# Kernel tuning notes

Hardware: AMD Instinct MI355X
Metric: run time of the kernel (lower is better)

## Reference

```python
import jax, jax.numpy as jnp
import numpy as np
from math import sqrt

NUM_HEADS = 16
DIM_MODEL = 1024


def setup_inputs() -> dict:
    key = jax.random.key(0)
    ks = jax.random.split(key, 12)
    B, S, D, M = 4, 1024, DIM_MODEL, 64
    bound = 1.0 / sqrt(D)
    def lin_w(k):
        return jax.random.uniform(k, (D, D), jnp.float32, -bound, bound)
    def lin_b(k):
        return jax.random.uniform(k, (D,), jnp.float32, -bound, bound)
    return {
        "query": jax.random.normal(ks[0], (B, S, D), jnp.float32),
        "key": jax.random.normal(ks[1], (B, S, D), jnp.float32),
        "value": jax.random.normal(ks[2], (B, S, D), jnp.float32),
        "mask": jax.random.randint(ks[3], (1, B, S, M), 0, 2).astype(jnp.float32),
        "Wq": lin_w(ks[4]), "bq": lin_b(ks[5]),
        "Wk": lin_w(ks[6]), "bk": lin_b(ks[7]),
        "Wv": lin_w(ks[8]), "bv": lin_b(ks[9]),
        "Wo": lin_w(ks[10]),
    }


def reference(query, key, value, mask, Wq, bq, Wk, bk, Wv, bv, Wo):
    B, S, D = query.shape
    H = NUM_HEADS
    d = D // H
    # projections + head split, permute(2,0,1,3) -> [H,B,S,d]
    q = (query @ Wq.T + bq).reshape(B, S, H, d).transpose(2, 0, 1, 3)
    k = (key @ Wk.T + bk).reshape(B, S, H, d).transpose(2, 0, 1, 3)
    v = (value @ Wv.T + bv).reshape(B, S, H, d).transpose(2, 0, 1, 3)
    attn = jnp.einsum("hbqd,hbkd->hbqk", q, k) / sqrt(d)  # [H,B,S,S]
    # custom mask: mask.repeat(H,1,1,1) then mask @ mask^T / sqrt(m).
    # Identical per-head, so compute once on [B,S,m] and broadcast over H.
    m2d = mask[0]  # [B,S,m]
    mm = jnp.einsum("bqm,bkm->bqk", m2d, m2d) / sqrt(m2d.shape[-1])
    attn = jnp.where(mm[None] == 0, jnp.float32(-1e9), attn)
    w = jax.nn.softmax(attn, axis=-1)  # dropout is identity in eval mode
    x = jnp.einsum("hbqk,hbkd->hbqd", w, v)  # [H,B,S,d]
    # torch: permute(1,2,0,3) -> [B,S,H,d]; transpose(1,2) -> [B,H,S,d];
    # contiguous().view(B,-1,H*d) -- row-major reshape (mixes head/seq layout, replicated faithfully)
    x = jnp.transpose(x, (1, 0, 2, 3))  # [B,H,S,d]
    x = x.reshape(B, -1, H * d)
    return x @ Wo.T
```

## Files before the change

### kernel.cpp

```cpp
#include <hip/hip_runtime.h>

typedef unsigned int u32;
typedef unsigned short u16;
typedef unsigned long long u64;
typedef __attribute__((ext_vector_type(8))) short s16x8;
typedef __attribute__((ext_vector_type(8))) __bf16 bf16x8;
typedef __attribute__((ext_vector_type(4))) float f32x4;
typedef __attribute__((ext_vector_type(16))) float f32x16;
typedef __attribute__((ext_vector_type(4))) u32 u32x4;

#define WSMB (1ull << 20)
#define QSC 0.18033688011112042f

static __device__ __forceinline__ u16 f2bf(float f) {
  u32 u = __builtin_bit_cast(u32, f);
  return (u16)((u + 0x7fffu + ((u >> 16) & 1u)) >> 16);
}

static __device__ __forceinline__ u32 pkbf(float lo, float hi) {
  u32 r;
  asm("v_cvt_pk_bf16_f32 %0, %1, %2" : "=v"(r) : "v"(lo), "v"(hi));
  return r;
}

static __device__ __forceinline__ float ex2(float x) {
  float r;
  asm("v_exp_f32 %0, %1" : "=v"(r) : "v"(x));
  return r;
}

static __device__ __forceinline__ f32x4 mfma16x16(s16x8 a, s16x8 b, f32x4 c) {
  return __builtin_amdgcn_mfma_f32_16x16x32_bf16(
      __builtin_bit_cast(bf16x8, a), __builtin_bit_cast(bf16x8, b), c, 0, 0, 0);
}

static __device__ __forceinline__ f32x16 mfma32x32(s16x8 a, s16x8 b, f32x16 c) {
  return __builtin_amdgcn_mfma_f32_32x32x16_bf16(
      __builtin_bit_cast(bf16x8, a), __builtin_bit_cast(bf16x8, b), c, 0, 0, 0);
}

#define GLOAD_LDS16(g, l)                                                      \
  __builtin_amdgcn_global_load_lds(                                            \
      (const __attribute__((address_space(1))) u32*)(const void*)(g),          \
      (__attribute__((address_space(3))) u32*)(void*)(l), 16, 0, 0)

__global__ __launch_bounds__(256) void k_cvt3(const float* __restrict__ a,
                                              const float* __restrict__ b,
                                              const float* __restrict__ c,
                                              u16* __restrict__ oa,
                                              u16* __restrict__ ob,
                                              u16* __restrict__ oc) {
  const float* s;
  u16* d;
  if (blockIdx.y == 0) { s = a; d = oa; }
  else if (blockIdx.y == 1) { s = b; d = ob; }
  else { s = c; d = oc; }
  int i = (blockIdx.x * 256 + threadIdx.x) * 4;
  float4 v = *(const float4*)(s + i);
  u64 p = (u64)f2bf(v.x) | ((u64)f2bf(v.y) << 16) | ((u64)f2bf(v.z) << 32) |
          ((u64)f2bf(v.w) << 48);
  *(u64*)(d + i) = p;
}

__global__ __launch_bounds__(256) void k_cvt4(const float* __restrict__ a,
                                              const float* __restrict__ b,
                                              const float* __restrict__ c,
                                              const float* __restrict__ e,
                                              u16* __restrict__ oa,
                                              u16* __restrict__ ob,
                                              u16* __restrict__ oc,
                                              u16* __restrict__ oe) {
  const float* s;
  u16* d;
  if (blockIdx.y == 0) { s = a; d = oa; }
  else if (blockIdx.y == 1) { s = b; d = ob; }
  else if (blockIdx.y == 2) { s = c; d = oc; }
  else { s = e; d = oe; }
  int i = (blockIdx.x * 256 + threadIdx.x) * 4;
  float4 v = *(const float4*)(s + i);
  u64 p = (u64)f2bf(v.x) | ((u64)f2bf(v.y) << 16) | ((u64)f2bf(v.z) << 32) |
          ((u64)f2bf(v.w) << 48);
  *(u64*)(d + i) = p;
}

__global__ __launch_bounds__(256) void k_bits(const float* __restrict__ mask,
                                              u64* __restrict__ bits) {
  int w = threadIdx.x >> 6, l = threadIdx.x & 63;
  int r = blockIdx.x * 4 + w;
  float v = mask[(size_t)r * 64 + l];
  u64 bl = __ballot(v != 0.0f);
  if (l == 0) bits[r] = bl;
}

__global__ __launch_bounds__(256) void k_mm(const u64* __restrict__ bits,
                                            u64* __restrict__ MB) {
  int wv = threadIdx.x >> 6, l = threadIdx.x & 63;
  int qg = blockIdx.x * 4 + wv;
  u64 bq = bits[qg];
  const u64* bb = bits + (qg & ~1023);
  u64* out = MB + (size_t)qg * 16;
  for (int kt = 0; kt < 16; kt++) {
    u64 bk = bb[kt * 64 + l];
    u64 m = __ballot((bq & bk) != 0ull);
    if (l == 0) out[kt] = m;
  }
}

static __device__ __forceinline__ void gemm_core(const u16* __restrict__ A,
                                                 const u16* __restrict__ Bw,
                                                 f32x4 (&acc)[4][4]) {
  __shared__ __attribute__((aligned(16))) u16 As[2][4096];
  __shared__ __attribute__((aligned(16))) u16 Bs[2][4096];
  const int t = threadIdx.x;
  const int l = t & 63, w = t >> 6, lr = l & 15, lk = l >> 4;
  const int amr = (w & 1) * 64, bnr = (w >> 1) * 64;
  const int c0 = t, c1 = t + 256;
  const int r0 = c0 >> 2, r1 = c1 >> 2;
  const int sw0 = ((c0 & 3) * 8) ^ ((r0 & 6) << 2);
  const int sw1 = ((c1 & 3) * 8) ^ ((r1 & 6) << 2);
  const u16* Ag0 = A + (size_t)r0 * 1024 + sw0;
  const u16* Ag1 = A + (size_t)r1 * 1024 + sw1;
  const u16* Bg0 = Bw + (size_t)r0 * 1024 + sw0;
  const u16* Bg1 = Bw + (size_t)r1 * 1024 + sw1;
  const int aswz = (lk * 16) ^ ((lr & 6) << 3);

  GLOAD_LDS16(Ag0, &As[0][c0 * 8]);
  GLOAD_LDS16(Ag1, &As[0][c1 * 8]);
  GLOAD_LDS16(Bg0, &Bs[0][c0 * 8]);
  GLOAD_LDS16(Bg1, &Bs[0][c1 * 8]);

  int cur = 0;
  for (int kt = 0; kt < 1024; kt += 32) {
    __syncthreads();
    if (kt < 992) {
      const int nxt = cur ^ 1;
      GLOAD_LDS16(Ag0 + kt + 32, &As[nxt][c0 * 8]);
      GLOAD_LDS16(Ag1 + kt + 32, &As[nxt][c1 * 8]);
      GLOAD_LDS16(Bg0 + kt + 32, &Bs[nxt][c0 * 8]);
      GLOAD_LDS16(Bg1 + kt + 32, &Bs[nxt][c1 * 8]);
    }
    const char* Ac = (const char*)As[cur];
    const char* Bc = (const char*)Bs[cur];
    s16x8 af[4], bf[4];
#pragma unroll
    for (int i = 0; i < 4; i++)
      af[i] = *(const s16x8*)(Ac + (amr + i * 16 + lr) * 64 + aswz);
#pragma unroll
    for (int j = 0; j < 4; j++)
      bf[j] = *(const s16x8*)(Bc + (bnr + j * 16 + lr) * 64 + aswz);
    __builtin_amdgcn_s_setprio(1);
#pragma unroll
    for (int i = 0; i < 4; i++)
#pragma unroll
      for (int j = 0; j < 4; j++)
        acc[i][j] = mfma16x16(af[i], bf[j], acc[i][j]);
    __builtin_amdgcn_s_setprio(0);
    cur ^= 1;
  }
}

__global__ __launch_bounds__(256) void k_qkv(
    const u16* __restrict__ Xq, const u16* __restrict__ Xk,
    const u16* __restrict__ Xv, const u16* __restrict__ Wqb,
    const u16* __restrict__ Wkb, const u16* __restrict__ Wvb,
    const float* __restrict__ bq, const float* __restrict__ bk,
    const float* __restrict__ bv, u16* __restrict__ Qo, u16* __restrict__ Ko,
    u16* __restrict__ V4) {
  const int bid0 = blockIdx.x;
  const int bid = (bid0 & 7) * 96 + (bid0 >> 3);
  const int proj = bid >> 8;
  const int rem = bid & 255;
  const int st = rem >> 3, dt = rem & 7;
  const u16* Xp = proj == 0 ? Xq : (proj == 1 ? Xk : Xv);
  const u16* Wp = proj == 0 ? Wqb : (proj == 1 ? Wkb : Wvb);
  const float* bias = proj == 0 ? bq : (proj == 1 ? bk : bv);
  const int t = threadIdx.x;
  const int l = t & 63, w = t >> 6, lr = l & 15, lk = l >> 4;
  const int amr = (w & 1) * 64, bnr = (w >> 1) * 64;
  f32x4 acc[4][4] = {};
  if (proj < 2) {
    const float sc = proj == 0 ? QSC : 1.0f;
    gemm_core(Wp + (size_t)dt * 131072, Xp + (size_t)st * 131072, acc);
    u16* O = proj ? Ko : Qo;
#pragma unroll
    for (int i = 0; i < 4; i++) {
      const int d0 = dt * 128 + amr + i * 16 + lk * 4;
      const int h = d0 >> 6, dd0 = d0 & 63;
      const float4 b4 = *(const float4*)(bias + d0);
#pragma unroll
      for (int j = 0; j < 4; j++) {
        const int s = st * 128 + bnr + j * 16 + lr;
        const int b_ = s >> 10, si = s & 1023;
        u32 e0 = pkbf((acc[i][j][0] + b4.x) * sc, (acc[i][j][1] + b4.y) * sc);
        u32 e1 = pkbf((acc[i][j][2] + b4.z) * sc, (acc[i][j][3] + b4.w) * sc);
        *(u64*)(O + ((size_t)((b_ * 16 + h) * 1024 + si)) * 64 + dd0) =
            (u64)e0 | ((u64)e1 << 32);
      }
    }
  } else {
    gemm_core(Xp + (size_t)st * 131072, Wp + (size_t)dt * 131072, acc);
#pragma unroll
    for (int i = 0; i < 4; i++) {
      const int s0 = st * 128 + amr + i * 16 + lk * 4;
      const int b_ = s0 >> 10, si = s0 & 1023;
      const int sblk = si >> 3, soff = si & 7;
#pragma unroll
      for (int j = 0; j < 4; j++) {
        const int d = dt * 128 + bnr + j * 16 + lr;
        const int h = d >> 6, dd = d & 63;
        const float bb = bias[d];
        u32 e0 = pkbf(acc[i][j][0] + bb, acc[i][j][1] + bb);
        u32 e1 = pkbf(acc[i][j][2] + bb, acc[i][j][3] + bb);
        *(u64*)(V4 + (size_t)(b_ * 16 + h) * 65536 +
                (size_t)(sblk * 64 + dd) * 8 + soff) =
            (u64)e0 | ((u64)e1 << 32);
      }
    }
  }
}

__global__ __launch_bounds__(256) void k_oproj(const u16* __restrict__ Xb,
                                               const u16* __restrict__ Wob,
                                               float* __restrict__ Out) {
  const int bid0 = blockIdx.x;
  const int bid = (bid0 & 7) * 32 + (bid0 >> 3);
  const int mb = bid >> 3, nb = bid & 7;
  f32x4 acc[4][4] = {};
  gemm_core(Xb + (size_t)mb * 131072, Wob + (size_t)nb * 131072, acc);
  const int t = threadIdx.x;
  const int l = t & 63, w = t >> 6, lr = l & 15, lk = l >> 4;
  const int amr = (w & 1) * 64, bnr = (w >> 1) * 64;
#pragma unroll
  for (int i = 0; i < 4; i++)
#pragma unroll
    for (int j = 0; j < 4; j++)
#pragma unroll
      for (int r = 0; r < 4; r++) {
        const int m = mb * 128 + amr + i * 16 + lk * 4 + r;
        const int n = nb * 128 + bnr + j * 16 + lr;
        Out[(size_t)m * 1024 + n] = acc[i][j][r];
      }
}

__global__ __launch_bounds__(256, 3) void k_attn(const u16* __restrict__ Qb,
                                                 const u16* __restrict__ Kb,
                                                 const u16* __restrict__ V4,
                                                 const u64* __restrict__ MB,
                                                 u16* __restrict__ xbuf) {
  __shared__ __attribute__((aligned(16))) u16 Ks[2][4096];
  __shared__ __attribute__((aligned(16))) u16 Vs[2][4096];
  const int t = threadIdx.x, l = t & 63, w = t >> 6;
  const int q5 = l & 31, hi = l >> 5;
  const int bid = (blockIdx.x & 7) * 64 + (blockIdx.x >> 3);
  const int qt = bid & 7, hb = bid >> 3;
  const int h = hb >> 2, b = hb & 3;
  const int s0 = qt * 128;
  const u16* Qhb = Qb + (size_t)(b * 16 + h) * 65536;
  const u16* Khb = Kb + (size_t)(b * 16 + h) * 65536;
  const u16* Vhb = V4 + (size_t)(b * 16 + h) * 65536;
  const int q = s0 + w * 32 + q5;
  const u64* MBq = MB + ((size_t)b * 1024 + q) * 16;

  s16x8 qf[4];
#pragma unroll
  for (int ds = 0; ds < 4; ds++)
    qf[ds] = *(const s16x8*)(Qhb + (size_t)q * 64 + ds * 16 + hi * 8);

  f32x16 xa0 = {}, xa1 = {};
  float ls = 0.f, m_ = -__builtin_inff();

  const int ca = t, cb_ = t + 256;
  const int rA = ca >> 3, colA = (ca & 7) * 16;
  const int rB = cb_ >> 3, colB = (cb_ & 7) * 16;
  const int sA = colA ^ ((rA & 7) << 4);
  const int sB = colB ^ ((rB & 7) << 4);
  const u16* KgA = Khb + (size_t)rA * 64 + (sA >> 1);
  const u16* KgB = Khb + (size_t)rB * 64 + (sB >> 1);
  const u16* VgA = Vhb + (size_t)(sA >> 4) * 512 + rA * 8;
  const u16* VgB = Vhb + (size_t)(sB >> 4) * 512 + rB * 8;

  const int rbase = q5 * 128 + ((hi * 16) ^ ((q5 & 7) << 4));

  GLOAD_LDS16(KgA, &Ks[0][ca * 8]);
  GLOAD_LDS16(KgB, &Ks[0][cb_ * 8]);
  GLOAD_LDS16(VgA, &Vs[0][ca * 8]);
  GLOAD_LDS16(VgB, &Vs[0][cb_ * 8]);
  u64 mw = MBq[0];

  int cur = 0;
  for (int kt = 0; kt < 16; kt++) {
    __syncthreads();
    if (kt < 15) {
      const int nxt = cur ^ 1;
      GLOAD_LDS16(KgA + (kt + 1) * 4096, &Ks[nxt][ca * 8]);
      GLOAD_LDS16(KgB + (kt + 1) * 4096, &Ks[nxt][cb_ * 8]);
      GLOAD_LDS16(VgA + (kt + 1) * 4096, &Vs[nxt][ca * 8]);
      GLOAD_LDS16(VgB + (kt + 1) * 4096, &Vs[nxt][cb_ * 8]);
    }
    const u64 nw = MBq[(kt + 1) & 15];
    const char* Kc = (const char*)Ks[cur];
    const char* Vc = (const char*)Vs[cur];

    f32x16 z0 = {}, z1 = {};
#pragma unroll
    for (int ds = 0; ds < 4; ds++) {
      s16x8 k0 = *(const s16x8*)(Kc + (rbase ^ (ds * 32)));
      s16x8 k1 = *(const s16x8*)(Kc + 4096 + (rbase ^ (ds * 32)));
      __builtin_amdgcn_s_setprio(1);
      z0 = mfma32x32(k0, qf[ds], z0);
      z1 = mfma32x32(k1, qf[ds], z1);
      __builtin_amdgcn_s_setprio(0);
    }

    float tmx[16];
#pragma unroll
    for (int r = 0; r < 16; r++) tmx[r] = fmaxf(z0[r], z1[r]);
#pragma unroll
    for (int st_ = 8; st_ >= 1; st_ >>= 1)
#pragma unroll
      for (int r = 0; r < 8; r++)
        if (r < st_) tmx[r] = fmaxf(tmx[r], tmx[r + st_]);
    float tm = tmx[0];
    tm = fmaxf(tm, __shfl_xor(tm, 32));
    if (tm > m_) {
      const float scl = ex2(m_ - tm);
      m_ = tm;
      ls *= scl;
      xa0 *= scl;
      xa1 *= scl;
    }

    float e0[16], e1[16];
#pragma unroll
    for (int r = 0; r < 16; r++) e0[r] = ex2(z0[r] - m_);
#pragma unroll
    for (int r = 0; r < 16; r++) e1[r] = ex2(z1[r] - m_);
    if (!__all(mw == ~0ull)) {
      const u32 mh0 = (u32)(mw >> (hi * 4));
      const u32 mh1 = (u32)(mw >> (hi * 4 + 32));
#pragma unroll
      for (int r = 0; r < 16; r++) {
        const int bp = 8 * (r >> 2) + (r & 3);
        e0[r] = ((mh0 >> bp) & 1u) ? e0[r] : 0.f;
        e1[r] = ((mh1 >> bp) & 1u) ? e1[r] : 0.f;
      }
    }
    float ts = 0.f;
#pragma unroll
    for (int r = 0; r < 16; r++) ts += e0[r] + e1[r];
    ls += ts;

    u32 P0[2][4], P1[2][4];
#pragma unroll
    for (int qi = 0; qi < 4; qi++) {
      P0[0][qi] = pkbf(e0[4 * qi], e0[4 * qi + 1]);
      P1[0][qi] = pkbf(e0[4 * qi + 2], e0[4 * qi + 3]);
      P0[1][qi] = pkbf(e1[4 * qi], e1[4 * qi + 1]);
      P1[1][qi] = pkbf(e1[4 * qi + 2], e1[4 * qi + 3]);
    }

#pragma unroll
    for (int ks = 0; ks < 4; ks++) {
      const int kb = ks >> 1, qi0 = (ks & 1) * 2, qi1 = qi0 + 1;
      u32 w0 = P0[kb][qi0], w2 = P0[kb][qi1];
      u32 w1 = P1[kb][qi0], w3 = P1[kb][qi1];
      asm("v_permlane32_swap_b32 %0, %1" : "+v"(w0), "+v"(w2));
      asm("v_permlane32_swap_b32 %0, %1" : "+v"(w1), "+v"(w3));
      u32x4 fv;
      fv[0] = w0; fv[1] = w1; fv[2] = w2; fv[3] = w3;
      const s16x8 pb = __builtin_bit_cast(s16x8, fv);
      s16x8 v0 = *(const s16x8*)(Vc + (rbase ^ (ks * 32)));
      s16x8 v1 = *(const s16x8*)(Vc + 4096 + (rbase ^ (ks * 32)));
      __builtin_amdgcn_s_setprio(1);
      xa0 = mfma32x32(v0, pb, xa0);
      xa1 = mfma32x32(v1, pb, xa1);
      __builtin_amdgcn_s_setprio(0);
    }
    mw = nw;
    cur ^= 1;
  }

  ls += __shfl_xor(ls, 32);
  const float inv = 1.0f / ls;
  const size_t rowb = (size_t)b * 1048576 + (size_t)(h * 64 + (q >> 4)) * 1024 +
                      (size_t)(q & 15) * 64;
#pragma unroll
  for (int qi = 0; qi < 4; qi++) {
    u32 a0 = pkbf(xa0[4 * qi] * inv, xa0[4 * qi + 1] * inv);
    u32 a1 = pkbf(xa0[4 * qi + 2] * inv, xa0[4 * qi + 3] * inv);
    *(u64*)(xbuf + rowb + 8 * qi + 4 * hi) = (u64)a0 | ((u64)a1 << 32);
    u32 b0 = pkbf(xa1[4 * qi] * inv, xa1[4 * qi + 1] * inv);
    u32 b1 = pkbf(xa1[4 * qi + 2] * inv, xa1[4 * qi + 3] * inv);
    *(u64*)(xbuf + rowb + 32 + 8 * qi + 4 * hi) = (u64)b0 | ((u64)b1 << 32);
  }
}

extern "C" void kernel_launch(void* const* d_in, const int* in_sizes, int n_in,
                              void* d_out, int out_size, void* d_ws,
                              size_t ws_size, hipStream_t stream) {
  const float* query = (const float*)d_in[0];
  const float* key_ = (const float*)d_in[1];
  const float* value = (const float*)d_in[2];
  const float* mask = (const float*)d_in[3];
  const float* bq = (const float*)d_in[5];
  const float* bk = (const float*)d_in[7];
  const float* bv = (const float*)d_in[9];
  const float* Wq = (const float*)d_in[4];
  const float* Wk = (const float*)d_in[6];
  const float* Wv = (const float*)d_in[8];
  const float* Wo = (const float*)d_in[10];

  char* ws = (char*)d_ws;
  u16* Xq = (u16*)(ws + 0 * WSMB);
  u16* Xk = (u16*)(ws + 8 * WSMB);
  u16* Xv = (u16*)(ws + 16 * WSMB);
  u16* Wqb = (u16*)(ws + 24 * WSMB);
  u16* Wkb = (u16*)(ws + 26 * WSMB);
  u16* Wvb = (u16*)(ws + 28 * WSMB);
  u16* Wob = (u16*)(ws + 30 * WSMB);
  u16* Qb = (u16*)(ws + 32 * WSMB);
  u16* Kb = (u16*)(ws + 40 * WSMB);
  u16* V4 = (u16*)(ws + 48 * WSMB);
  u64* bits = (u64*)(ws + 56 * WSMB);
  u64* MBm = (u64*)(ws + 8 * WSMB);
  u16* xbuf = Xq;

  k_cvt3<<<dim3(4096, 3), 256, 0, stream>>>(query, key_, value, Xq, Xk, Xv);
  k_cvt4<<<dim3(1024, 4), 256, 0, stream>>>(Wq, Wk, Wv, Wo, Wqb, Wkb, Wvb, Wob);
  k_bits<<<1024, 256, 0, stream>>>(mask, bits);
  k_qkv<<<768, 256, 0, stream>>>(Xq, Xk, Xv, Wqb, Wkb, Wvb, bq, bk, bv, Qb, Kb,
                                 V4);
  k_mm<<<1024, 256, 0, stream>>>(bits, MBm);
  k_attn<<<512, 256, 0, stream>>>(Qb, Kb, V4, MBm, xbuf);
  k_oproj<<<256, 256, 0, stream>>>(xbuf, Wob, (float*)d_out);
}
```

Measured before the change: 119.0 us.

## Merge conversion kernels into one launch and halve attention block query tile

The three preprocessing kernels (activation cast, weight cast, mask bit packing) become a single launch over a 2D grid, with out-of-range blocks exiting early. This removes two kernel launches. The attention kernel now uses 128-thread blocks covering 64 queries each, launched over 1024 blocks, which doubles the block count to spread work more evenly across CUs. Each thread issues four K and four V async loads per tile instead of two, and the K/V tiles are fetched twice as often overall, raising L2 traffic.

New measurement: 120.7 us. About the same (+1.4%).

```diff
diff --git a/kernel.cpp b/kernel.cpp
--- a/kernel.cpp
+++ b/kernel.cpp
@@ -44,52 +44,40 @@
       (const __attribute__((address_space(1))) u32*)(const void*)(g),          \
       (__attribute__((address_space(3))) u32*)(void*)(l), 16, 0, 0)
 
-__global__ __launch_bounds__(256) void k_cvt3(const float* __restrict__ a,
-                                              const float* __restrict__ b,
-                                              const float* __restrict__ c,
-                                              u16* __restrict__ oa,
-                                              u16* __restrict__ ob,
-                                              u16* __restrict__ oc) {
+__global__ __launch_bounds__(256) void k_prep(
+    const float* __restrict__ xq, const float* __restrict__ xk,
+    const float* __restrict__ xv, const float* __restrict__ wq,
+    const float* __restrict__ wk, const float* __restrict__ wv,
+    const float* __restrict__ wo, const float* __restrict__ mask,
+    u16* __restrict__ oxq, u16* __restrict__ oxk, u16* __restrict__ oxv,
+    u16* __restrict__ owq, u16* __restrict__ owk, u16* __restrict__ owv,
+    u16* __restrict__ owo, u64* __restrict__ bits) {
+  const int y = blockIdx.y;
+  if (y >= 3 && blockIdx.x >= 1024) return;
+  if (y == 7) {
+    int w = threadIdx.x >> 6, l = threadIdx.x & 63;
+    int r = blockIdx.x * 4 + w;
+    float v = mask[(size_t)r * 64 + l];
+    u64 bl = __ballot(v != 0.0f);
+    if (l == 0) bits[r] = bl;
+    return;
+  }
   const float* s;
   u16* d;
-  if (blockIdx.y == 0) { s = a; d = oa; }
-  else if (blockIdx.y == 1) { s = b; d = ob; }
-  else { s = c; d = oc; }
+  switch (y) {
+    case 0: s = xq; d = oxq; break;
+    case 1: s = xk; d = oxk; break;
+    case 2: s = xv; d = oxv; break;
+    case 3: s = wq; d = owq; break;
+    case 4: s = wk; d = owk; break;
+    case 5: s = wv; d = owv; break;
+    default: s = wo; d = owo; break;
+  }
   int i = (blockIdx.x * 256 + threadIdx.x) * 4;
   float4 v = *(const float4*)(s + i);
   u64 p = (u64)f2bf(v.x) | ((u64)f2bf(v.y) << 16) | ((u64)f2bf(v.z) << 32) |
           ((u64)f2bf(v.w) << 48);
   *(u64*)(d + i) = p;
-}
-
-__global__ __launch_bounds__(256) void k_cvt4(const float* __restrict__ a,
-                                              const float* __restrict__ b,
-                                              const float* __restrict__ c,
-                                              const float* __restrict__ e,
-                                              u16* __restrict__ oa,
-                                              u16* __restrict__ ob,
-                                              u16* __restrict__ oc,
-                                              u16* __restrict__ oe) {
-  const float* s;
-  u16* d;
-  if (blockIdx.y == 0) { s = a; d = oa; }
-  else if (blockIdx.y == 1) { s = b; d = ob; }
-  else if (blockIdx.y == 2) { s = c; d = oc; }
-  else { s = e; d = oe; }
-  int i = (blockIdx.x * 256 + threadIdx.x) * 4;
-  float4 v = *(const float4*)(s + i);
-  u64 p = (u64)f2bf(v.x) | ((u64)f2bf(v.y) << 16) | ((u64)f2bf(v.z) << 32) |
-          ((u64)f2bf(v.w) << 48);
-  *(u64*)(d + i) = p;
-}
-
-__global__ __launch_bounds__(256) void k_bits(const float* __restrict__ mask,
-                                              u64* __restrict__ bits) {
-  int w = threadIdx.x >> 6, l = threadIdx.x & 63;
-  int r = blockIdx.x * 4 + w;
-  float v = mask[(size_t)r * 64 + l];
-  u64 bl = __ballot(v != 0.0f);
-  if (l == 0) bits[r] = bl;
 }
 
 __global__ __launch_bounds__(256) void k_mm(const u64* __restrict__ bits,
@@ -242,7 +230,7 @@
       }
 }
 
-__global__ __launch_bounds__(256, 3) void k_attn(const u16* __restrict__ Qb,
+__global__ __launch_bounds__(128, 2) void k_attn(const u16* __restrict__ Qb,
                                                  const u16* __restrict__ Kb,
                                                  const u16* __restrict__ V4,
                                                  const u64* __restrict__ MB,
@@ -251,10 +239,10 @@
   __shared__ __attribute__((aligned(16))) u16 Vs[2][4096];
   const int t = threadIdx.x, l = t & 63, w = t >> 6;
   const int q5 = l & 31, hi = l >> 5;
-  const int bid = (blockIdx.x & 7) * 64 + (blockIdx.x >> 3);
-  const int qt = bid & 7, hb = bid >> 3;
+  const int bid = (blockIdx.x & 7) * 128 + (blockIdx.x >> 3);
+  const int qt = bid & 15, hb = bid >> 4;
   const int h = hb >> 2, b = hb & 3;
-  const int s0 = qt * 128;
+  const int s0 = qt * 64;
   const u16* Qhb = Qb + (size_t)(b * 16 + h) * 65536;
   const u16* Khb = Kb + (size_t)(b * 16 + h) * 65536;
   const u16* Vhb = V4 + (size_t)(b * 16 + h) * 65536;
@@ -269,22 +257,25 @@
   f32x16 xa0 = {}, xa1 = {};
   float ls = 0.f, m_ = -__builtin_inff();
 
-  const int ca = t, cb_ = t + 256;
-  const int rA = ca >> 3, colA = (ca & 7) * 16;
-  const int rB = cb_ >> 3, colB = (cb_ & 7) * 16;
-  const int sA = colA ^ ((rA & 7) << 4);
-  const int sB = colB ^ ((rB & 7) << 4);
-  const u16* KgA = Khb + (size_t)rA * 64 + (sA >> 1);
-  const u16* KgB = Khb + (size_t)rB * 64 + (sB >> 1);
-  const u16* VgA = Vhb + (size_t)(sA >> 4) * 512 + rA * 8;
-  const u16* VgB = Vhb + (size_t)(sB >> 4) * 512 + rB * 8;
+  const u16 *Kg[4], *Vg[4];
+  int cdst[4];
+#pragma unroll
+  for (int i = 0; i < 4; i++) {
+    const int c = t + i * 128;
+    const int r_ = c >> 3, col = (c & 7) * 16;
+    const int s_ = col ^ ((r_ & 7) << 4);
+    Kg[i] = Khb + (size_t)r_ * 64 + (s_ >> 1);
+    Vg[i] = Vhb + (size_t)(s_ >> 4) * 512 + r_ * 8;
+    cdst[i] = c * 8;
+  }
 
   const int rbase = q5 * 128 + ((hi * 16) ^ ((q5 & 7) << 4));
 
-  GLOAD_LDS16(KgA, &Ks[0][ca * 8]);
-  GLOAD_LDS16(KgB, &Ks[0][cb_ * 8]);
-  GLOAD_LDS16(VgA, &Vs[0][ca * 8]);
-  GLOAD_LDS16(VgB, &Vs[0][cb_ * 8]);
+#pragma unroll
+  for (int i = 0; i < 4; i++) {
+    GLOAD_LDS16(Kg[i], &Ks[0][cdst[i]]);
+    GLOAD_LDS16(Vg[i], &Vs[0][cdst[i]]);
+  }
   u64 mw = MBq[0];
 
   int cur = 0;
@@ -292,10 +283,11 @@
     __syncthreads();
     if (kt < 15) {
       const int nxt = cur ^ 1;
-      GLOAD_LDS16(KgA + (kt + 1) * 4096, &Ks[nxt][ca * 8]);
-      GLOAD_LDS16(KgB + (kt + 1) * 4096, &Ks[nxt][cb_ * 8]);
-      GLOAD_LDS16(VgA + (kt + 1) * 4096, &Vs[nxt][ca * 8]);
-      GLOAD_LDS16(VgB + (kt + 1) * 4096, &Vs[nxt][cb_ * 8]);
+#pragma unroll
+      for (int i = 0; i < 4; i++) {
+        GLOAD_LDS16(Kg[i] + (kt + 1) * 4096, &Ks[nxt][cdst[i]]);
+        GLOAD_LDS16(Vg[i] + (kt + 1) * 4096, &Vs[nxt][cdst[i]]);
+      }
     }
     const u64 nw = MBq[(kt + 1) & 15];
     const char* Kc = (const char*)Ks[cur];
@@ -425,12 +417,12 @@
   u64* MBm = (u64*)(ws + 8 * WSMB);
   u16* xbuf = Xq;
 
-  k_cvt3<<<dim3(4096, 3), 256, 0, stream>>>(query, key_, value, Xq, Xk, Xv);
-  k_cvt4<<<dim3(1024, 4), 256, 0, stream>>>(Wq, Wk, Wv, Wo, Wqb, Wkb, Wvb, Wob);
-  k_bits<<<1024, 256, 0, stream>>>(mask, bits);
+  k_prep<<<dim3(4096, 8), 256, 0, stream>>>(query, key_, value, Wq, Wk, Wv, Wo,
+                                            mask, Xq, Xk, Xv, Wqb, Wkb, Wvb,
+                                            Wob, bits);
   k_qkv<<<768, 256, 0, stream>>>(Xq, Xk, Xv, Wqb, Wkb, Wvb, bq, bk, bv, Qb, Kb,
                                  V4);
   k_mm<<<1024, 256, 0, stream>>>(bits, MBm);
-  k_attn<<<512, 256, 0, stream>>>(Qb, Kb, V4, MBm, xbuf);
+  k_attn<<<1024, 128, 0, stream>>>(Qb, Kb, V4, MBm, xbuf);
   k_oproj<<<256, 256, 0, stream>>>(xbuf, Wob, (float*)d_out);
 }
```
